# Optimization experiments

Measured on AMD Instinct MI355X. Metric: run time of the kernel, lower is better.

## Reference

```python
import jax, jax.numpy as jnp
import numpy as np

L, B, S, H = 4, 2, 2048, 1024
NH, HD, FFN = 16, 64, 4096
EPS = 1e-5


def setup_inputs() -> dict:
    key = jax.random.key(0)
    ks = jax.random.split(key, 6)
    std = 0.02
    return {
        "hidden_states": jax.random.normal(ks[0], (B, S, H), jnp.float32),
        "ln1_g": jnp.ones((L, H), jnp.float32),
        "ln1_b": jnp.zeros((L, H), jnp.float32),
        "Wqkv": jax.random.normal(ks[1], (L, H, 3 * H), jnp.float32) * std,
        "Wproj": jax.random.normal(ks[2], (L, H, H), jnp.float32) * std,
        "ln2_g": jnp.ones((L, H), jnp.float32),
        "ln2_b": jnp.zeros((L, H), jnp.float32),
        "Wfc1": jax.random.normal(ks[3], (L, H, FFN), jnp.float32) * std,
        "Wfc2": jax.random.normal(ks[4], (L, FFN, H), jnp.float32) * std,
        "lnf_g": jnp.ones((H,), jnp.float32),
        "lnf_b": jnp.zeros((H,), jnp.float32),
    }


def _layernorm(x, g, b):
    mu = jnp.mean(x, axis=-1, keepdims=True)
    var = jnp.mean(jnp.square(x - mu), axis=-1, keepdims=True)
    return (x - mu) * jax.lax.rsqrt(var + EPS) * g + b


def _block_forward(x, ln1_g, ln1_b, Wqkv, Wproj, ln2_g, ln2_b, Wfc1, Wfc2, lnf_g, lnf_b):
    scale = HD ** -0.5
    causal = jnp.tril(jnp.ones((S, S), bool))  # [S, S]

    def layer(x, p):
        g1, b1, wqkv, wproj, g2, b2, wfc1, wfc2 = p
        # Attention sub-block (pre-norm)
        h = _layernorm(x, g1, b1)
        qkv = (h @ wqkv).reshape(B, S, 3, NH, HD)
        q, k, v = qkv[:, :, 0], qkv[:, :, 1], qkv[:, :, 2]  # [B,S,NH,HD]
        scores = jnp.einsum("bqhd,bkhd->bhqk", q, k) * scale
        scores = jnp.where(causal, scores, -jnp.inf)
        probs = jax.nn.softmax(scores, axis=-1)
        attn = jnp.einsum("bhqk,bkhd->bqhd", probs, v).reshape(B, S, H)
        x = x + attn @ wproj
        # FFN sub-block (pre-norm)
        h = _layernorm(x, g2, b2)
        h = jax.nn.gelu(h @ wfc1, approximate=False) @ wfc2
        return x + h, None

    x, _ = jax.lax.scan(layer, x, (ln1_g, ln1_b, Wqkv, Wproj, ln2_g, ln2_b, Wfc1, Wfc2))
    return _layernorm(x, lnf_g, lnf_b)


def reference(hidden_states, ln1_g, ln1_b, Wqkv, Wproj, ln2_g, ln2_b, Wfc1, Wfc2, lnf_g, lnf_b):
    return _block_forward(hidden_states, ln1_g, ln1_b, Wqkv, Wproj, ln2_g, ln2_b, Wfc1, Wfc2, lnf_g, lnf_b)
```

## Files before the change

kernel.cpp:

```cpp
#include <hip/hip_runtime.h>
#include <hip/hip_bf16.h>
#include <math.h>

#define LYRS 4
#define BB   2
#define SS   2048
#define HH   1024
#define NHD  16
#define HDD  64
#define FFN_ 4096
#define BS   (BB*SS)
#define EPS_ 1e-5f

typedef __attribute__((ext_vector_type(8))) __bf16 bf16x8;
typedef __attribute__((ext_vector_type(4))) __bf16 bf16x4;
typedef __attribute__((ext_vector_type(4))) float f32x4;
typedef __attribute__((address_space(1))) void* gas_t;
typedef __attribute__((address_space(3))) void* las_t;

__device__ inline void async16(void* lds, const void* g) {
    __builtin_amdgcn_global_load_lds((gas_t)g, (las_t)lds, 16, 0, 0);
}

__device__ inline void storev(float* p, float v) { *p = v; }
__device__ inline void storev(__hip_bfloat16* p, float v) { *p = __float2bfloat16(v); }

template <typename OutT>
__global__ void ln_k(const float* __restrict__ x, const float* __restrict__ g,
                     const float* __restrict__ b, OutT* __restrict__ y) {
    const int row = blockIdx.x;
    const int tid = threadIdx.x;
    const float* xr = x + (size_t)row * HH;

    float v[4];
    float s = 0.f, s2 = 0.f;
#pragma unroll
    for (int i = 0; i < 4; ++i) {
        v[i] = xr[tid + i * 256];
        s  += v[i];
        s2 += v[i] * v[i];
    }
#pragma unroll
    for (int o = 1; o < 64; o <<= 1) {
        s  += __shfl_xor(s,  o);
        s2 += __shfl_xor(s2, o);
    }
    __shared__ float sh[8];
    const int wave = tid >> 6, lane = tid & 63;
    if (lane == 0) { sh[wave] = s; sh[4 + wave] = s2; }
    __syncthreads();
    if (tid == 0) {
        float ts  = sh[0] + sh[1] + sh[2] + sh[3];
        float ts2 = sh[4] + sh[5] + sh[6] + sh[7];
        float mu  = ts * (1.f / HH);
        sh[0] = mu;
        sh[1] = ts2 * (1.f / HH) - mu * mu;
    }
    __syncthreads();
    const float mu   = sh[0];
    const float rstd = rsqrtf(sh[1] + EPS_);
#pragma unroll
    for (int i = 0; i < 4; ++i) {
        int c = tid + i * 256;
        storev(&y[(size_t)row * HH + c], (v[i] - mu) * rstd * g[c] + b[c]);
    }
}

__global__ __launch_bounds__(256) void transpose_cast(const float* __restrict__ W,
                                                      __hip_bfloat16* __restrict__ WT,
                                                      int K, int N) {
    __shared__ float t[32][33];
    const int n0 = blockIdx.x * 32, k0 = blockIdx.y * 32;
    const int tx = threadIdx.x & 31, ty8 = threadIdx.x >> 5;
#pragma unroll
    for (int i = 0; i < 4; ++i) {
        int k = ty8 + i * 8;
        t[k][tx] = W[(size_t)(k0 + k) * N + n0 + tx];
    }
    __syncthreads();
#pragma unroll
    for (int i = 0; i < 4; ++i) {
        int n = ty8 + i * 8;
        WT[(size_t)(n0 + n) * K + k0 + tx] = __float2bfloat16(t[tx][n]);
    }
}

template <bool GELU, bool RES, int SPLITK, typename OutT>
__global__ __launch_bounds__(256) void gemm_bf16(
    const __hip_bfloat16* __restrict__ A,
    const __hip_bfloat16* __restrict__ BT,
    const float* __restrict__ R,
    OutT* __restrict__ C,
    int M, int N, int K)
{
    __shared__ unsigned short As[2][128 * 32];
    __shared__ unsigned short Bs[2][128 * 32];

    const int tid  = threadIdx.x;
    const int lane = tid & 63;
    const int wv   = tid >> 6;
    const int wy   = wv >> 1, wx = wv & 1;
    const int nby  = M >> 7;
    const int tiles = nby * (N >> 7);
    const int ks   = blockIdx.x / tiles;
    const int rem  = blockIdx.x % tiles;
    const int by   = rem % nby;
    const int bx   = rem / nby;
    const int row0 = by * 128;
    const int col0 = bx * 128;
    const int lm   = lane & 15;
    const int kq   = lane >> 4;

    const int Kslice = K / SPLITK;
    const int kbeg   = ks * Kslice;
    const int nsteps = Kslice >> 5;

    const unsigned short* Ag = (const unsigned short*)A;
    const unsigned short* Bg = (const unsigned short*)BT;

    const int li0 = tid, li1 = 256 + tid;
    const int r0 = li0 >> 2, c0 = (li0 & 3) << 3;
    const int r1 = li1 >> 2, c1 = (li1 & 3) << 3;
    const unsigned short* Ag0 = Ag + (size_t)(row0 + r0) * K + c0;
    const unsigned short* Ag1 = Ag + (size_t)(row0 + r1) * K + c1;
    const unsigned short* Bg0 = Bg + (size_t)(col0 + r0) * K + c0;
    const unsigned short* Bg1 = Bg + (size_t)(col0 + r1) * K + c1;

    auto stage = [&](int buf, int k) {
        async16(&As[buf][li0 * 8], Ag0 + k);
        async16(&As[buf][li1 * 8], Ag1 + k);
        async16(&Bs[buf][li0 * 8], Bg0 + k);
        async16(&Bs[buf][li1 * 8], Bg1 + k);
    };

    f32x4 acc[4][4] = {};

    stage(0, kbeg);
    __syncthreads();

    for (int s = 0; s < nsteps; ++s) {
        const int buf = s & 1;
        if (s + 1 < nsteps) stage(buf ^ 1, kbeg + ((s + 1) << 5));

        bf16x8 af[4], bfr[4];
#pragma unroll
        for (int i = 0; i < 4; ++i)
            af[i] = *(const bf16x8*)&As[buf][(wy * 64 + i * 16 + lm) * 32 + kq * 8];
#pragma unroll
        for (int j = 0; j < 4; ++j)
            bfr[j] = *(const bf16x8*)&Bs[buf][(wx * 64 + j * 16 + lm) * 32 + kq * 8];
#pragma unroll
        for (int i = 0; i < 4; ++i)
#pragma unroll
            for (int j = 0; j < 4; ++j)
                acc[i][j] = __builtin_amdgcn_mfma_f32_16x16x32_bf16(
                    af[i], bfr[j], acc[i][j], 0, 0, 0);

        __syncthreads();
    }

#pragma unroll
    for (int i = 0; i < 4; ++i) {
#pragma unroll
        for (int j = 0; j < 4; ++j) {
            int gc = col0 + wx * 64 + j * 16 + lm;
#pragma unroll
            for (int r = 0; r < 4; ++r) {
                int gr = row0 + wy * 64 + i * 16 + kq * 4 + r;
                float v = acc[i][j][r];
                if constexpr (SPLITK > 1) {
                    atomicAdd((float*)&C[(size_t)gr * N + gc], v);
                } else {
                    if (RES)  v += R[(size_t)gr * N + gc];
                    if (GELU) v = 0.5f * v * (1.0f + erff(v * 0.70710678118654752f));
                    storev(&C[(size_t)gr * N + gc], v);
                }
            }
        }
    }
}

__global__ __launch_bounds__(256) void attn_fa3(const __bf16* __restrict__ qkv,
                                                __bf16* __restrict__ out) {
    __shared__ __bf16 Ks[2][64 * 72];
    __shared__ __bf16 Vt[2][64 * 72];
    __shared__ __bf16 Ps[4][2][16 * 72];

    const int tid  = threadIdx.x;
    const int lane = tid & 63;
    const int w    = tid >> 6;
    const int lm   = lane & 15;
    const int kq   = lane >> 4;

    const int x  = blockIdx.x;
    const int bh = x & 31;
    const int h  = bh & 15;
    const int b  = bh >> 4;
    const int a  = (x >> 5) & 7;
    const int qt = (x & 256) ? (15 - a) : a;
    const int q0 = qt * 128;

    const size_t rs   = 3 * HH;
    const size_t base = (size_t)b * SS * rs + (size_t)h * HDD;

    const int krow0 = tid >> 3,        kc0 = (tid & 7) << 3;
    const int krow1 = (256 + tid) >> 3, kc1 = ((256 + tid) & 7) << 3;
    const int vkey  = tid & 63;
    const int vcb0  = (tid >> 6) << 3, vcb1 = ((256 + tid) >> 6) << 3;

    bf16x8 qf[2][2];
#pragma unroll
    for (int s = 0; s < 2; ++s)
#pragma unroll
        for (int kh = 0; kh < 2; ++kh) {
            bf16x8 t = *(const bf16x8*)&qkv[base +
                (size_t)(q0 + w * 32 + s * 16 + lm) * rs + kh * 32 + kq * 8];
#pragma unroll
            for (int j = 0; j < 8; ++j) t[j] = (__bf16)((float)t[j] * 0.125f);
            qf[s][kh] = t;
        }

    f32x4 ot[2][4] = {};
    float m_i[2] = {-INFINITY, -INFINITY};
    float l_i[2] = {0.f, 0.f};

    const int qmax_w = q0 + w * 32 + 31;
    const int ktmax  = (q0 + 127) >> 6;

    bf16x8 kr0, kr1, vr0, vr1;
    {
        const int k0 = 0;
        kr0 = *(const bf16x8*)&qkv[base + (size_t)(k0 + krow0) * rs + HH + kc0];
        kr1 = *(const bf16x8*)&qkv[base + (size_t)(k0 + krow1) * rs + HH + kc1];
        vr0 = *(const bf16x8*)&qkv[base + (size_t)(k0 + vkey) * rs + 2 * HH + vcb0];
        vr1 = *(const bf16x8*)&qkv[base + (size_t)(k0 + vkey) * rs + 2 * HH + vcb1];
        *(bf16x8*)&Ks[0][krow0 * 72 + kc0] = kr0;
        *(bf16x8*)&Ks[0][krow1 * 72 + kc1] = kr1;
#pragma unroll
        for (int j = 0; j < 8; ++j) Vt[0][(vcb0 + j) * 72 + vkey] = vr0[j];
#pragma unroll
        for (int j = 0; j < 8; ++j) Vt[0][(vcb1 + j) * 72 + vkey] = vr1[j];
    }
    __syncthreads();

    for (int kt = 0; kt <= ktmax; ++kt) {
        const int k0  = kt << 6;
        const int buf = kt & 1;

        if (kt < ktmax) {
            const int kn = k0 + 64;
            kr0 = *(const bf16x8*)&qkv[base + (size_t)(kn + krow0) * rs + HH + kc0];
            kr1 = *(const bf16x8*)&qkv[base + (size_t)(kn + krow1) * rs + HH + kc1];
            vr0 = *(const bf16x8*)&qkv[base + (size_t)(kn + vkey) * rs + 2 * HH + vcb0];
            vr1 = *(const bf16x8*)&qkv[base + (size_t)(kn + vkey) * rs + 2 * HH + vcb1];
        }

        if (k0 <= qmax_w) {
#pragma unroll
            for (int s = 0; s < 2; ++s) {
                f32x4 st[4] = {};
#pragma unroll
                for (int kh = 0; kh < 2; ++kh)
#pragma unroll
                    for (int m = 0; m < 4; ++m) {
                        bf16x8 kf = *(const bf16x8*)&Ks[buf][(m * 16 + lm) * 72 + kh * 32 + kq * 8];
                        st[m] = __builtin_amdgcn_mfma_f32_16x16x32_bf16(
                            kf, qf[s][kh], st[m], 0, 0, 0);
                    }

                const int qg = q0 + w * 32 + s * 16 + lm;
                if (k0 + 63 > q0 + w * 32 + s * 16) {
#pragma unroll
                    for (int m = 0; m < 4; ++m) {
                        int keyb = k0 + m * 16 + kq * 4;
#pragma unroll
                        for (int r = 0; r < 4; ++r)
                            if (keyb + r > qg) st[m][r] = -INFINITY;
                    }
                }

                float mloc = -INFINITY;
#pragma unroll
                for (int m = 0; m < 4; ++m)
#pragma unroll
                    for (int r = 0; r < 4; ++r) mloc = fmaxf(mloc, st[m][r]);
                mloc = fmaxf(mloc, __shfl_xor(mloc, 16));
                mloc = fmaxf(mloc, __shfl_xor(mloc, 32));
                float mn    = fmaxf(m_i[s], mloc);
                float alpha = __expf(m_i[s] - mn);
                m_i[s] = mn;

                float sum = 0.f;
#pragma unroll
                for (int m = 0; m < 4; ++m) {
                    bf16x4 pb;
#pragma unroll
                    for (int r = 0; r < 4; ++r) {
                        float p = __expf(st[m][r] - mn);
                        sum += p;
                        pb[r] = (__bf16)p;
                    }
                    *(bf16x4*)&Ps[w][s][lm * 72 + m * 16 + kq * 4] = pb;
                }
                sum += __shfl_xor(sum, 16);
                sum += __shfl_xor(sum, 32);
                l_i[s] = l_i[s] * alpha + sum;

#pragma unroll
                for (int dt = 0; dt < 4; ++dt) ot[s][dt] *= alpha;

#pragma unroll
                for (int kh = 0; kh < 2; ++kh) {
                    bf16x8 pf = *(const bf16x8*)&Ps[w][s][lm * 72 + kh * 32 + kq * 8];
#pragma unroll
                    for (int dt = 0; dt < 4; ++dt) {
                        bf16x8 vf = *(const bf16x8*)&Vt[buf][(dt * 16 + lm) * 72 + kh * 32 + kq * 8];
                        ot[s][dt] = __builtin_amdgcn_mfma_f32_16x16x32_bf16(
                            vf, pf, ot[s][dt], 0, 0, 0);
                    }
                }
            }
        }

        if (kt < ktmax) {
            const int nb = buf ^ 1;
            *(bf16x8*)&Ks[nb][krow0 * 72 + kc0] = kr0;
            *(bf16x8*)&Ks[nb][krow1 * 72 + kc1] = kr1;
#pragma unroll
            for (int j = 0; j < 8; ++j) Vt[nb][(vcb0 + j) * 72 + vkey] = vr0[j];
#pragma unroll
            for (int j = 0; j < 8; ++j) Vt[nb][(vcb1 + j) * 72 + vkey] = vr1[j];
            __syncthreads();
        }
    }

#pragma unroll
    for (int s = 0; s < 2; ++s) {
        float inv = 1.f / l_i[s];
        int qg = q0 + w * 32 + s * 16 + lm;
#pragma unroll
        for (int dt = 0; dt < 4; ++dt) {
            bf16x4 ob;
#pragma unroll
            for (int r = 0; r < 4; ++r) ob[r] = (__bf16)(ot[s][dt][r] * inv);
            *(bf16x4*)&out[(size_t)(b * SS + qg) * HH + h * HDD + dt * 16 + kq * 4] = ob;
        }
    }
}

extern "C" void kernel_launch(void* const* d_in, const int* in_sizes, int n_in,
                              void* d_out, int out_size, void* d_ws, size_t ws_size,
                              hipStream_t stream) {
    const float* hidden = (const float*)d_in[0];
    const float* ln1_g  = (const float*)d_in[1];
    const float* ln1_b  = (const float*)d_in[2];
    const float* Wqkv   = (const float*)d_in[3];
    const float* Wproj  = (const float*)d_in[4];
    const float* ln2_g  = (const float*)d_in[5];
    const float* ln2_b  = (const float*)d_in[6];
    const float* Wfc1   = (const float*)d_in[7];
    const float* Wfc2   = (const float*)d_in[8];
    const float* lnf_g  = (const float*)d_in[9];
    const float* lnf_b  = (const float*)d_in[10];

    float* x = (float*)d_out;

    char* p = (char*)d_ws;
    __hip_bfloat16* hbuf  = (__hip_bfloat16*)p; p += (size_t)BS * HH * 2;
    __hip_bfloat16* qkvb  = (__hip_bfloat16*)p; p += (size_t)BS * 3 * HH * 2;
    __hip_bfloat16* attnb = (__hip_bfloat16*)p; p += (size_t)BS * HH * 2;
    __hip_bfloat16* ffnb  = (__hip_bfloat16*)p; p += (size_t)BS * FFN_ * 2;
    __hip_bfloat16* wqkvT = (__hip_bfloat16*)p; p += (size_t)3 * HH * HH * 2;
    __hip_bfloat16* wprojT= (__hip_bfloat16*)p; p += (size_t)HH * HH * 2;
    __hip_bfloat16* wfc1T = (__hip_bfloat16*)p; p += (size_t)FFN_ * HH * 2;
    __hip_bfloat16* wfc2T = (__hip_bfloat16*)p; p += (size_t)HH * FFN_ * 2;

    hipMemcpyAsync(x, hidden, (size_t)BS * HH * sizeof(float),
                   hipMemcpyDeviceToDevice, stream);

    const int NBY = BS / 128;

    for (int lyr = 0; lyr < LYRS; ++lyr) {
        transpose_cast<<<dim3(3 * HH / 32, HH / 32), 256, 0, stream>>>(
            Wqkv + (size_t)lyr * HH * 3 * HH, wqkvT, HH, 3 * HH);
        transpose_cast<<<dim3(HH / 32, HH / 32), 256, 0, stream>>>(
            Wproj + (size_t)lyr * HH * HH, wprojT, HH, HH);
        transpose_cast<<<dim3(FFN_ / 32, HH / 32), 256, 0, stream>>>(
            Wfc1 + (size_t)lyr * HH * FFN_, wfc1T, HH, FFN_);
        transpose_cast<<<dim3(HH / 32, FFN_ / 32), 256, 0, stream>>>(
            Wfc2 + (size_t)lyr * FFN_ * HH, wfc2T, FFN_, HH);

        ln_k<__hip_bfloat16><<<BS, 256, 0, stream>>>(
            x, ln1_g + lyr * HH, ln1_b + lyr * HH, hbuf);
        gemm_bf16<false, false, 1, __hip_bfloat16>
            <<<(3 * HH / 128) * NBY, 256, 0, stream>>>(
            hbuf, wqkvT, nullptr, qkvb, BS, 3 * HH, HH);
        attn_fa3<<<512, 256, 0, stream>>>((const __bf16*)qkvb, (__bf16*)attnb);
        gemm_bf16<false, true, 1, float>
            <<<(HH / 128) * NBY, 256, 0, stream>>>(
            attnb, wprojT, x, x, BS, HH, HH);
        ln_k<__hip_bfloat16><<<BS, 256, 0, stream>>>(
            x, ln2_g + lyr * HH, ln2_b + lyr * HH, hbuf);
        gemm_bf16<true, false, 1, __hip_bfloat16>
            <<<(FFN_ / 128) * NBY, 256, 0, stream>>>(
            hbuf, wfc1T, nullptr, ffnb, BS, FFN_, HH);
        gemm_bf16<false, false, 2, float>
            <<<(HH / 128) * NBY * 2, 256, 0, stream>>>(
            ffnb, wfc2T, nullptr, x, BS, HH, FFN_);
    }
    ln_k<float><<<BS, 256, 0, stream>>>(x, lnf_g, lnf_b, x);
}
```

Measured before the change: 1.277 ms.

## Triple-buffer GEMM LDS staging and XOR-swizzle tiles to avoid bank conflicts

```diff
diff --git a/kernel.cpp b/kernel.cpp
--- a/kernel.cpp
+++ b/kernel.cpp
@@ -93,8 +93,8 @@
     OutT* __restrict__ C,
     int M, int N, int K)
 {
-    __shared__ unsigned short As[2][128 * 32];
-    __shared__ unsigned short Bs[2][128 * 32];
+    __shared__ unsigned short As[3][128 * 32];
+    __shared__ unsigned short Bs[3][128 * 32];
 
     const int tid  = threadIdx.x;
     const int lane = tid & 63;
@@ -119,12 +119,15 @@
     const unsigned short* Bg = (const unsigned short*)BT;
 
     const int li0 = tid, li1 = 256 + tid;
-    const int r0 = li0 >> 2, c0 = (li0 & 3) << 3;
-    const int r1 = li1 >> 2, c1 = (li1 & 3) << 3;
-    const unsigned short* Ag0 = Ag + (size_t)(row0 + r0) * K + c0;
-    const unsigned short* Ag1 = Ag + (size_t)(row0 + r1) * K + c1;
-    const unsigned short* Bg0 = Bg + (size_t)(col0 + r0) * K + c0;
-    const unsigned short* Bg1 = Bg + (size_t)(col0 + r1) * K + c1;
+    const int r0 = li0 >> 2, r1 = li1 >> 2;
+    const int g0 = (r0 & 3) ^ ((r0 >> 2) & 1);
+    const int g1 = (r1 & 3) ^ ((r1 >> 2) & 1);
+    const int sc0 = (((li0 & 3) ^ g0) << 3);
+    const int sc1 = (((li1 & 3) ^ g1) << 3);
+    const unsigned short* Ag0 = Ag + (size_t)(row0 + r0) * K + sc0;
+    const unsigned short* Ag1 = Ag + (size_t)(row0 + r1) * K + sc1;
+    const unsigned short* Bg0 = Bg + (size_t)(col0 + r0) * K + sc0;
+    const unsigned short* Bg1 = Bg + (size_t)(col0 + r1) * K + sc1;
 
     auto stage = [&](int buf, int k) {
         async16(&As[buf][li0 * 8], Ag0 + k);
@@ -133,22 +136,30 @@
         async16(&Bs[buf][li1 * 8], Bg1 + k);
     };
 
+    const int rdoff = ((kq ^ (lm & 3) ^ ((lm >> 2) & 1)) << 3);
+
     f32x4 acc[4][4] = {};
 
     stage(0, kbeg);
-    __syncthreads();
-
+    if (nsteps > 1) stage(1, kbeg + 32);
+
+    int bufi = 0;
+    int nxti = 2;
     for (int s = 0; s < nsteps; ++s) {
-        const int buf = s & 1;
-        if (s + 1 < nsteps) stage(buf ^ 1, kbeg + ((s + 1) << 5));
+        if (s + 2 < nsteps) stage(nxti, kbeg + ((s + 2) << 5));
+
+        if (s + 2 < nsteps)      asm volatile("s_waitcnt vmcnt(16)" ::: "memory");
+        else if (s + 1 < nsteps) asm volatile("s_waitcnt vmcnt(8)"  ::: "memory");
+        else                     asm volatile("s_waitcnt vmcnt(0)"  ::: "memory");
+        __builtin_amdgcn_s_barrier();
 
         bf16x8 af[4], bfr[4];
 #pragma unroll
         for (int i = 0; i < 4; ++i)
-            af[i] = *(const bf16x8*)&As[buf][(wy * 64 + i * 16 + lm) * 32 + kq * 8];
+            af[i] = *(const bf16x8*)&As[bufi][(wy * 64 + i * 16 + lm) * 32 + rdoff];
 #pragma unroll
         for (int j = 0; j < 4; ++j)
-            bfr[j] = *(const bf16x8*)&Bs[buf][(wx * 64 + j * 16 + lm) * 32 + kq * 8];
+            bfr[j] = *(const bf16x8*)&Bs[bufi][(wx * 64 + j * 16 + lm) * 32 + rdoff];
 #pragma unroll
         for (int i = 0; i < 4; ++i)
 #pragma unroll
@@ -156,7 +167,11 @@
                 acc[i][j] = __builtin_amdgcn_mfma_f32_16x16x32_bf16(
                     af[i], bfr[j], acc[i][j], 0, 0, 0);
 
-        __syncthreads();
+        asm volatile("s_waitcnt lgkmcnt(0)" ::: "memory");
+        __builtin_amdgcn_s_barrier();
+
+        bufi = (bufi == 2) ? 0 : bufi + 1;
+        nxti = (nxti == 2) ? 0 : nxti + 1;
     }
 
 #pragma unroll
```

Result: no change. 1.285 ms (+0.6%).

## Add 256x256-tile GEMM for FFN layers and split-K the projection GEMM

Applied to the files above, without the earlier changes.

```diff
diff --git a/kernel.cpp b/kernel.cpp
--- a/kernel.cpp
+++ b/kernel.cpp
@@ -180,6 +180,105 @@
     }
 }
 
+template <bool GELU, bool RES, int SPLITK, typename OutT>
+__global__ __launch_bounds__(512, 2) void gemm256(
+    const __hip_bfloat16* __restrict__ A,
+    const __hip_bfloat16* __restrict__ BT,
+    const float* __restrict__ R,
+    OutT* __restrict__ C,
+    int M, int N, int K)
+{
+    __shared__ unsigned short As[2][256 * 32];
+    __shared__ unsigned short Bs[2][256 * 32];
+
+    const int tid  = threadIdx.x;
+    const int lane = tid & 63;
+    const int wv   = tid >> 6;
+    const int wy   = wv >> 2;
+    const int wx   = wv & 3;
+    const int nby  = M >> 8;
+    const int tiles = nby * (N >> 8);
+    const int ks   = blockIdx.x / tiles;
+    const int rem  = blockIdx.x % tiles;
+    const int by   = rem % nby;
+    const int bx   = rem / nby;
+    const int row0 = by * 256;
+    const int col0 = bx * 256;
+    const int lm   = lane & 15;
+    const int kq   = lane >> 4;
+
+    const int Kslice = K / SPLITK;
+    const int kbeg   = ks * Kslice;
+    const int nsteps = Kslice >> 5;
+
+    const unsigned short* Ag = (const unsigned short*)A;
+    const unsigned short* Bg = (const unsigned short*)BT;
+
+    const int liA = tid, liB = 512 + tid;
+    const int ra = liA >> 2, rb = liB >> 2;
+    const int ca = ((liA & 3) ^ ((ra >> 1) & 3)) << 3;
+    const int cb = ((liB & 3) ^ ((rb >> 1) & 3)) << 3;
+    const unsigned short* Ag0 = Ag + (size_t)(row0 + ra) * K + ca;
+    const unsigned short* Ag1 = Ag + (size_t)(row0 + rb) * K + cb;
+    const unsigned short* Bg0 = Bg + (size_t)(col0 + ra) * K + ca;
+    const unsigned short* Bg1 = Bg + (size_t)(col0 + rb) * K + cb;
+
+    auto stage = [&](int buf, int k) {
+        async16(&As[buf][liA * 8], Ag0 + k);
+        async16(&As[buf][liB * 8], Ag1 + k);
+        async16(&Bs[buf][liA * 8], Bg0 + k);
+        async16(&Bs[buf][liB * 8], Bg1 + k);
+    };
+
+    const int rdoff = ((kq ^ ((lm >> 1) & 3)) << 3);
+
+    f32x4 acc[8][4] = {};
+
+    stage(0, kbeg);
+    __syncthreads();
+
+    for (int s = 0; s < nsteps; ++s) {
+        const int buf = s & 1;
+        if (s + 1 < nsteps) stage(buf ^ 1, kbeg + ((s + 1) << 5));
+
+        bf16x8 af[8], bfr[4];
+#pragma unroll
+        for (int i = 0; i < 8; ++i)
+            af[i] = *(const bf16x8*)&As[buf][(wy * 128 + i * 16 + lm) * 32 + rdoff];
+#pragma unroll
+        for (int j = 0; j < 4; ++j)
+            bfr[j] = *(const bf16x8*)&Bs[buf][(wx * 64 + j * 16 + lm) * 32 + rdoff];
+#pragma unroll
+        for (int i = 0; i < 8; ++i)
+#pragma unroll
+            for (int j = 0; j < 4; ++j)
+                acc[i][j] = __builtin_amdgcn_mfma_f32_16x16x32_bf16(
+                    af[i], bfr[j], acc[i][j], 0, 0, 0);
+
+        __syncthreads();
+    }
+
+#pragma unroll
+    for (int i = 0; i < 8; ++i) {
+#pragma unroll
+        for (int j = 0; j < 4; ++j) {
+            int gc = col0 + wx * 64 + j * 16 + lm;
+#pragma unroll
+            for (int r = 0; r < 4; ++r) {
+                int gr = row0 + wy * 128 + i * 16 + kq * 4 + r;
+                float v = acc[i][j][r];
+                if constexpr (SPLITK > 1) {
+                    atomicAdd((float*)&C[(size_t)gr * N + gc], v);
+                } else {
+                    if (RES)  v += R[(size_t)gr * N + gc];
+                    if (GELU) v = 0.5f * v * (1.0f + erff(v * 0.70710678118654752f));
+                    storev(&C[(size_t)gr * N + gc], v);
+                }
+            }
+        }
+    }
+}
+
 __global__ __launch_bounds__(256) void attn_fa3(const __bf16* __restrict__ qkv,
                                                 __bf16* __restrict__ out) {
     __shared__ __bf16 Ks[2][64 * 72];
@@ -396,16 +495,16 @@
             <<<(3 * HH / 128) * NBY, 256, 0, stream>>>(
             hbuf, wqkvT, nullptr, qkvb, BS, 3 * HH, HH);
         attn_fa3<<<512, 256, 0, stream>>>((const __bf16*)qkvb, (__bf16*)attnb);
-        gemm_bf16<false, true, 1, float>
-            <<<(HH / 128) * NBY, 256, 0, stream>>>(
-            attnb, wprojT, x, x, BS, HH, HH);
+        gemm_bf16<false, false, 2, float>
+            <<<(HH / 128) * NBY * 2, 256, 0, stream>>>(
+            attnb, wprojT, nullptr, x, BS, HH, HH);
         ln_k<__hip_bfloat16><<<BS, 256, 0, stream>>>(
             x, ln2_g + lyr * HH, ln2_b + lyr * HH, hbuf);
-        gemm_bf16<true, false, 1, __hip_bfloat16>
-            <<<(FFN_ / 128) * NBY, 256, 0, stream>>>(
+        gemm256<true, false, 1, __hip_bfloat16>
+            <<<(BS / 256) * (FFN_ / 256), 512, 0, stream>>>(
             hbuf, wfc1T, nullptr, ffnb, BS, FFN_, HH);
-        gemm_bf16<false, false, 2, float>
-            <<<(HH / 128) * NBY * 2, 256, 0, stream>>>(
+        gemm256<false, false, 4, float>
+            <<<(BS / 256) * (HH / 256) * 4, 512, 0, stream>>>(
             ffnb, wfc2T, nullptr, x, BS, HH, FFN_);
     }
     ln_k<float><<<BS, 256, 0, stream>>>(x, lnf_g, lnf_b, x);
```

After: 1.518 ms. +18.9%, slower.
